# Performance work log

Measured on AMD Instinct MI355X. Metric: run time of the kernel, lower is better.

The kernel has to match this reference:

```python
import jax, jax.numpy as jnp
from jax import lax
import numpy as np

B, T, F, U = 256, 150, 1024, 28


def setup_inputs() -> dict:
    key = jax.random.key(0)
    ks = jax.random.split(key, 10)
    s = 0.05  # keep tanh/sigmoid unsaturated, ~glorot magnitude
    return {
        "x": jax.random.normal(ks[0], (B, T, F), jnp.float32),
        "Wa": jax.random.normal(ks[1], (U, F), jnp.float32) * s,
        "Ua": jax.random.normal(ks[2], (F, F), jnp.float32) * s,
        "Va": jax.random.normal(ks[3], (F, 1), jnp.float32) * s,
        "Ba1": jax.random.normal(ks[4], (1, F), jnp.float32) * s,
        "Ba2": jax.random.normal(ks[5], (1, F), jnp.float32) * s,
        "Ba3": jax.random.normal(ks[6], (1, 1), jnp.float32) * s,
        "gru_kernel": jax.random.normal(ks[7], (F, 3 * U), jnp.float32) * s,
        "gru_rkernel": jax.random.normal(ks[8], (U, 3 * U), jnp.float32) * s,
        "gru_bias": jax.random.normal(ks[9], (2, 3 * U), jnp.float32) * s,
    }


def reference(x, Wa, Ua, Va, Ba1, Ba2, Ba3, gru_kernel, gru_rkernel, gru_bias):
    b, t, f = x.shape
    u = Wa.shape[0]
    # UaH is loop-invariant in the original (x @ Ua + Ba2 each step) -> hoist it.
    UaH = jnp.einsum('btf,fg->btg', x, Ua) + Ba2  # (B,T,F)

    def step(h, _):
        # Bahdanau attention conditioned on previous GRU state h (B,U)
        WaS = h @ Wa + Ba1                                    # (B,F)
        scores = jnp.einsum('btf,fo->bt', jnp.tanh(UaH + WaS[:, None, :]), Va) + Ba3[0, 0]
        a = jax.nn.softmax(scores, axis=1)                    # (B,T)
        ctx = jnp.einsum('btf,bt->bf', x, a)                  # (B,F)
        # Keras GRUCell (reset_after=True)
        xz = ctx @ gru_kernel + gru_bias[0]                   # (B,3U)
        hz = h @ gru_rkernel + gru_bias[1]                    # (B,3U)
        x_z, x_r, x_h = jnp.split(xz, 3, axis=-1)
        r_z, r_r, r_h = jnp.split(hz, 3, axis=-1)
        z = jax.nn.sigmoid(x_z + r_z)
        r = jax.nn.sigmoid(x_r + r_r)
        hh = jnp.tanh(x_h + r * r_h)
        h_new = z * h + (1.0 - z) * hh
        return h_new, h_new

    h0 = jnp.zeros((b, u), x.dtype)
    _, ys = lax.scan(step, h0, None, length=t)  # (T,B,U)
    return jnp.transpose(ys, (1, 0, 2))         # (B,T,U)
```

## Files before the change

### kernel.cpp

```cpp
#include <hip/hip_runtime.h>
#include <hip/hip_bf16.h>


typedef _Float16 h8 __attribute__((ext_vector_type(8)));
typedef _Float16 h4 __attribute__((ext_vector_type(4)));
typedef _Float16 h2 __attribute__((ext_vector_type(2)));
typedef float    f4 __attribute__((ext_vector_type(4)));
typedef float    f2 __attribute__((ext_vector_type(2)));

#define B_   256
#define T_   150
#define F_   1024
#define U_   28
#define TU3  84

__device__ __forceinline__ float fast_exp(float x) {
    return __builtin_amdgcn_exp2f(x * 1.4426950408889634f);
}
__device__ __forceinline__ float fast_tanh(float x) {
    float e = __builtin_amdgcn_exp2f(x * 2.8853900817779268f);
    float r = __builtin_amdgcn_rcpf(e + 1.0f);
    return 1.0f - 2.0f * r;
}
__device__ __forceinline__ float fast_sigmoid(float x) {
    float e = __builtin_amdgcn_exp2f(-x * 1.4426950408889634f);
    return __builtin_amdgcn_rcpf(1.0f + e);
}

__global__ void k_cvt(const float* __restrict__ in, _Float16* __restrict__ out, int n4) {
    int i = blockIdx.x * blockDim.x + threadIdx.x;
    int stride = gridDim.x * blockDim.x;
    const f4* in4 = (const f4*)in;
    h4* out4 = (h4*)out;
    for (; i < n4; i += stride) {
        f4 v = in4[i];
        h4 o;
        o[0] = (_Float16)v[0]; o[1] = (_Float16)v[1];
        o[2] = (_Float16)v[2]; o[3] = (_Float16)v[3];
        out4[i] = o;
    }
}

__global__ void k_cvt_transpose(const float* __restrict__ in, _Float16* __restrict__ out) {
    int idx = blockIdx.x * blockDim.x + threadIdx.x;
    int r = idx >> 10, c = idx & 1023;
    out[(c << 10) + r] = (_Float16)in[idx];
}

#define BM 128
#define BN 128
#define BK 32
#define LDT 40

__global__ __launch_bounds__(256) void k_gemm(
    const _Float16* __restrict__ A,
    const _Float16* __restrict__ Bt,
    const float*    __restrict__ bias,
    _Float16*       __restrict__ C)
{
    __shared__ _Float16 As[BM][LDT];
    __shared__ _Float16 Bs[BN][LDT];
    const int K = 1024;
    int bm = blockIdx.y, bn = blockIdx.x;
    int tid = threadIdx.x;
    int lane = tid & 63, wid = tid >> 6;
    int wm = wid >> 1, wn = wid & 1;
    f4 acc[4][4];
#pragma unroll
    for (int i = 0; i < 4; i++)
#pragma unroll
        for (int j = 0; j < 4; j++) { f4 z = {0.f, 0.f, 0.f, 0.f}; acc[i][j] = z; }

    int row0 = bm * BM, col0 = bn * BN;
    for (int kt = 0; kt < K; kt += BK) {
#pragma unroll
        for (int p = 0; p < 2; ++p) {
            int s = tid + p * 256;
            int r = s >> 2, seg = s & 3;
            h8 va = *(const h8*)(A  + (size_t)(row0 + r) * K + kt + seg * 8);
            *(h8*)(&As[r][seg * 8]) = va;
            h8 vb = *(const h8*)(Bt + (size_t)(col0 + r) * K + kt + seg * 8);
            *(h8*)(&Bs[r][seg * 8]) = vb;
        }
        __syncthreads();
        int kq = (lane >> 4) * 8;
        h8 af[4], bf[4];
#pragma unroll
        for (int mi = 0; mi < 4; mi++) af[mi] = *(const h8*)(&As[wm * 64 + mi * 16 + (lane & 15)][kq]);
#pragma unroll
        for (int ni = 0; ni < 4; ni++) bf[ni] = *(const h8*)(&Bs[wn * 64 + ni * 16 + (lane & 15)][kq]);
#pragma unroll
        for (int mi = 0; mi < 4; mi++)
#pragma unroll
            for (int ni = 0; ni < 4; ni++)
                acc[mi][ni] = __builtin_amdgcn_mfma_f32_16x16x32_f16(af[mi], bf[ni], acc[mi][ni], 0, 0, 0);
        __syncthreads();
    }
    int rq = (lane >> 4) * 4, cq = lane & 15;
#pragma unroll
    for (int mi = 0; mi < 4; mi++)
#pragma unroll
        for (int ni = 0; ni < 4; ni++) {
            int gc = col0 + wn * 64 + ni * 16 + cq;
            float bv = bias[gc];
#pragma unroll
            for (int j = 0; j < 4; j++) {
                int gr = row0 + wm * 64 + mi * 16 + rq + j;
                C[(size_t)gr * 1024 + gc] = (_Float16)(acc[mi][ni][j] + bv);
            }
        }
}

#define XLD 72

__global__ __launch_bounds__(256) void k_gemm_xg(
    const _Float16* __restrict__ A,
    const float*    __restrict__ gk,
    _Float16*       __restrict__ C)
{
    __shared__ _Float16 As[128][XLD];
    __shared__ _Float16 Bs[96][XLD];
    int tid = threadIdx.x;
    int lane = tid & 63, wid = tid >> 6;
    int wm = wid >> 1, wn = wid & 1;
    int row0 = blockIdx.x * 128;
    f4 acc[4][3];
#pragma unroll
    for (int i = 0; i < 4; i++)
#pragma unroll
        for (int j = 0; j < 3; j++) { f4 z = {0.f, 0.f, 0.f, 0.f}; acc[i][j] = z; }

    if (tid < 432) { h2 z; z[0] = (_Float16)0.f; z[1] = (_Float16)0.f; ((h2*)&Bs[84][0])[tid] = z; }

    for (int kt = 0; kt < 1024; kt += 64) {
#pragma unroll
        for (int p = 0; p < 4; ++p) {
            int s = tid + p * 256;
            int r = s >> 3, seg = s & 7;
            *(h8*)(&As[r][seg * 8]) = *(const h8*)(A + (size_t)(row0 + r) * 1024 + kt + seg * 8);
        }
#pragma unroll
        for (int p = 0; p < 21; ++p) {
            int s = tid + p * 256;
            int j = s % 84, k = s / 84;
            Bs[j][k] = (_Float16)gk[(size_t)(kt + k) * 84 + j];
        }
        __syncthreads();
#pragma unroll
        for (int kk = 0; kk < 64; kk += 32) {
            int kq = kk + (lane >> 4) * 8;
            h8 af[4], bf[3];
#pragma unroll
            for (int mi = 0; mi < 4; mi++) af[mi] = *(const h8*)(&As[wm * 64 + mi * 16 + (lane & 15)][kq]);
#pragma unroll
            for (int ni = 0; ni < 3; ni++) bf[ni] = *(const h8*)(&Bs[wn * 48 + ni * 16 + (lane & 15)][kq]);
#pragma unroll
            for (int mi = 0; mi < 4; mi++)
#pragma unroll
                for (int ni = 0; ni < 3; ni++)
                    acc[mi][ni] = __builtin_amdgcn_mfma_f32_16x16x32_f16(af[mi], bf[ni], acc[mi][ni], 0, 0, 0);
        }
        __syncthreads();
    }
    int rq = (lane >> 4) * 4, cq = lane & 15;
#pragma unroll
    for (int mi = 0; mi < 4; mi++)
#pragma unroll
        for (int ni = 0; ni < 3; ni++) {
            int gc = wn * 48 + ni * 16 + cq;
            if (gc < 84) {
#pragma unroll
                for (int j = 0; j < 4; j++) {
                    int gr = row0 + wm * 64 + mi * 16 + rq + j;
                    C[(size_t)gr * 84 + gc] = (_Float16)acc[mi][ni][j];
                }
            }
        }
}

__global__ __launch_bounds__(1024) void k_recur2(
    const _Float16* __restrict__ uah,
    const _Float16* __restrict__ xg,
    const float* __restrict__ Wa,
    const float* __restrict__ Va,
    const float* __restrict__ Ba1,
    const float* __restrict__ grk,
    const float* __restrict__ gbias,
    float* __restrict__ out)
{
    __shared__ _Float16 sWa[U_ * F_];
    __shared__ _Float16 sXG[T_ * TU3];
    __shared__ float sWaS[F_];
    __shared__ float sScore[160];
    __shared__ float sPart[8 * TU3];
    __shared__ float sGrk[U_ * TU3];
    __shared__ float sHz[TU3];
    __shared__ float sH[U_];

    int b = blockIdx.x;
    int tid = threadIdx.x;
    int lane = tid & 63, wvid = tid >> 6;

    for (int i = tid; i < U_ * F_; i += 1024) sWa[i] = (_Float16)Wa[i];
    {
        const _Float16* xgb = xg + (size_t)b * T_ * TU3;
        for (int i = tid; i < T_ * TU3; i += 1024) sXG[i] = xgb[i];
    }
    for (int i = tid; i < U_ * TU3; i += 1024) sGrk[i] = grk[i];
    if (tid < U_) sH[tid] = 0.f;

    float rBa1 = Ba1[tid];
    float rV0[8], rV1[8];
    {
        f4 a0 = *(const f4*)(Va + 8 * lane);
        f4 a1 = *(const f4*)(Va + 8 * lane + 4);
        f4 b0 = *(const f4*)(Va + 512 + 8 * lane);
        f4 b1 = *(const f4*)(Va + 512 + 8 * lane + 4);
#pragma unroll
        for (int e = 0; e < 4; ++e) { rV0[e] = a0[e]; rV0[4 + e] = a1[e]; rV1[e] = b0[e]; rV1[4 + e] = b1[e]; }
    }
    int p4c = tid / TU3, p4j = tid - p4c * TU3;
    bool p4on = tid < 8 * TU3;
    bool hzon = (tid >= 896) && (tid < 896 + TU3);
    int hj = tid - 896;
    float rGb1 = hzon ? gbias[TU3 + hj] : 0.f;
    float rG0 = 0.f, rG1 = 0.f, rG2 = 0.f;
    if (tid < U_) { rG0 = gbias[tid]; rG1 = gbias[U_ + tid]; rG2 = gbias[2 * U_ + tid]; }
    __syncthreads();

    const _Float16* ub = uah + (size_t)b * T_ * F_;
    float* ob = out + (size_t)b * T_ * U_;

    for (int t = 0; t < T_; ++t) {
        {
            float acc = rBa1;
#pragma unroll
            for (int u = 0; u < U_; ++u) acc += sH[u] * (float)sWa[u * F_ + tid];
            sWaS[tid] = acc;
        }
        __syncthreads();
        float rW0[8], rW1[8];
        {
            f4 a0 = *(const f4*)(sWaS + 8 * lane);
            f4 a1 = *(const f4*)(sWaS + 8 * lane + 4);
            f4 b0 = *(const f4*)(sWaS + 512 + 8 * lane);
            f4 b1 = *(const f4*)(sWaS + 512 + 8 * lane + 4);
#pragma unroll
            for (int e = 0; e < 4; ++e) { rW0[e] = a0[e]; rW0[4 + e] = a1[e]; rW1[e] = b0[e]; rW1[4 + e] = b1[e]; }
        }
        {
            int r = wvid;
            const h8* pr = (const h8*)(ub + (size_t)r * F_);
            h8 u0 = pr[lane], u1 = pr[64 + lane];
            while (r < T_) {
                int rn = r + 16;
                h8 n0, n1;
                if (rn < T_) {
                    const h8* pn = (const h8*)(ub + (size_t)rn * F_);
                    n0 = pn[lane]; n1 = pn[64 + lane];
                }
                float acc = 0.f;
#pragma unroll
                for (int e = 0; e < 8; ++e) {
                    float s0 = (float)u0[e] + rW0[e];
                    acc += fast_tanh(s0) * rV0[e];
                    float s1 = (float)u1[e] + rW1[e];
                    acc += fast_tanh(s1) * rV1[e];
                }
#pragma unroll
                for (int off = 32; off; off >>= 1) acc += __shfl_xor(acc, off, 64);
                if (lane == 0) sScore[r] = acc;
                u0 = n0; u1 = n1; r = rn;
            }
        }
        __syncthreads();
        if (wvid == 0) {
            float v0 = (lane < T_)       ? sScore[lane]       : -1e30f;
            float v1 = (lane + 64 < T_)  ? sScore[lane + 64]  : -1e30f;
            float v2 = (lane + 128 < T_) ? sScore[lane + 128] : -1e30f;
            float m = fmaxf(v0, fmaxf(v1, v2));
#pragma unroll
            for (int off = 32; off; off >>= 1) m = fmaxf(m, __shfl_xor(m, off, 64));
            float e0 = (lane < T_)       ? fast_exp(v0 - m) : 0.f;
            float e1 = (lane + 64 < T_)  ? fast_exp(v1 - m) : 0.f;
            float e2 = (lane + 128 < T_) ? fast_exp(v2 - m) : 0.f;
            float s = e0 + e1 + e2;
#pragma unroll
            for (int off = 32; off; off >>= 1) s += __shfl_xor(s, off, 64);
            float rs = __builtin_amdgcn_rcpf(s);
            if (lane < T_)       sScore[lane]       = e0 * rs;
            if (lane + 64 < T_)  sScore[lane + 64]  = e1 * rs;
            if (lane + 128 < T_) sScore[lane + 128] = e2 * rs;
        }
        __syncthreads();
        if (p4on) {
            float acc = 0.f;
            for (int r = p4c; r < T_; r += 8) acc += sScore[r] * (float)sXG[r * TU3 + p4j];
            sPart[p4c * TU3 + p4j] = acc;
        }
        if (hzon) {
            float hz = rGb1;
#pragma unroll
            for (int u = 0; u < U_; ++u) hz += sH[u] * sGrk[u * TU3 + hj];
            sHz[hj] = hz;
        }
        __syncthreads();
        if (tid < U_) {
            float x0 = rG0, x1 = rG1, x2 = rG2;
#pragma unroll
            for (int c = 0; c < 8; ++c) {
                x0 += sPart[c * TU3 + tid];
                x1 += sPart[c * TU3 + U_ + tid];
                x2 += sPart[c * TU3 + 2 * U_ + tid];
            }
            float z  = fast_sigmoid(x0 + sHz[tid]);
            float r  = fast_sigmoid(x1 + sHz[U_ + tid]);
            float hh = fast_tanh(x2 + r * sHz[2 * U_ + tid]);
            float hn = z * sH[tid] + (1.f - z) * hh;
            sH[tid] = hn;
            ob[(size_t)t * U_ + tid] = hn;
        }
        __syncthreads();
    }
}

extern "C" void kernel_launch(void* const* d_in, const int* in_sizes, int n_in,
                              void* d_out, int out_size, void* d_ws, size_t ws_size,
                              hipStream_t stream) {
    (void)in_sizes; (void)n_in; (void)out_size; (void)ws_size;
    const float* x   = (const float*)d_in[0];
    const float* Wa  = (const float*)d_in[1];
    const float* Ua  = (const float*)d_in[2];
    const float* Va  = (const float*)d_in[3];
    const float* Ba1 = (const float*)d_in[4];
    const float* Ba2 = (const float*)d_in[5];
    const float* gk  = (const float*)d_in[7];
    const float* grk = (const float*)d_in[8];
    const float* gb  = (const float*)d_in[9];
    float* out = (float*)d_out;

    const size_t NX = (size_t)B_ * T_ * F_;
    _Float16* xh  = (_Float16*)d_ws;
    _Float16* uat = xh + NX;
    _Float16* uah = uat + (size_t)F_ * F_;
    _Float16* xgh = uah + NX;

    k_cvt<<<2048, 256, 0, stream>>>(x, xh, (int)(NX / 4));
    k_cvt_transpose<<<(F_ * F_) / 256, 256, 0, stream>>>(Ua, uat);
    dim3 gg(F_ / BN, (B_ * T_) / BM);
    k_gemm<<<gg, 256, 0, stream>>>(xh, uat, Ba2, uah);
    k_gemm_xg<<<(B_ * T_) / 128, 256, 0, stream>>>(xh, gk, xgh);
    k_recur2<<<B_, 1024, 0, stream>>>(uah, xgh, Wa, Va, Ba1, grk, gb, out);
}
```

Before: 2.667 ms.

## Fold tanh constants into scores and defer softmax normalization past context reduction

The attention score loop now rewrites tanh·Va as a constant sum minus 2·Va·rcp(exp2+1), with the 2·log2e scale folded into WaS and Va, which trims per-element arithmetic in the hot loop. Softmax drops its max subtraction and separate normalization pass: each score is exponentiated directly, the denominator is summed by a spare wavefront in parallel with the context reduction, and the 1/sum scale is applied to the final small vector. This removes a full barrier phase per timestep. Without max subtraction, exp can overflow if scores grow large, which relies on scores staying bounded.

Measured after the change: 2.231 ms. -16.4%, faster.

```diff
diff --git a/kernel.cpp b/kernel.cpp
--- a/kernel.cpp
+++ b/kernel.cpp
@@ -14,17 +14,20 @@
 #define U_   28
 #define TU3  84
 
+#define C2LOG2E 2.8853900817779268f
+#define LOG2E   1.4426950408889634f
+
 __device__ __forceinline__ float fast_exp(float x) {
-    return __builtin_amdgcn_exp2f(x * 1.4426950408889634f);
+    return __builtin_amdgcn_exp2f(x * LOG2E);
+}
+__device__ __forceinline__ float fast_sigmoid(float x) {
+    float e = __builtin_amdgcn_exp2f(-x * LOG2E);
+    return __builtin_amdgcn_rcpf(1.0f + e);
 }
 __device__ __forceinline__ float fast_tanh(float x) {
-    float e = __builtin_amdgcn_exp2f(x * 2.8853900817779268f);
+    float e = __builtin_amdgcn_exp2f(x * C2LOG2E);
     float r = __builtin_amdgcn_rcpf(e + 1.0f);
     return 1.0f - 2.0f * r;
-}
-__device__ __forceinline__ float fast_sigmoid(float x) {
-    float e = __builtin_amdgcn_exp2f(-x * 1.4426950408889634f);
-    return __builtin_amdgcn_rcpf(1.0f + e);
 }
 
 __global__ void k_cvt(const float* __restrict__ in, _Float16* __restrict__ out, int n4) {
@@ -196,6 +199,7 @@
     __shared__ float sGrk[U_ * TU3];
     __shared__ float sHz[TU3];
     __shared__ float sH[U_];
+    __shared__ float sDen;
 
     int b = blockIdx.x;
     int tid = threadIdx.x;
@@ -210,17 +214,22 @@
     if (tid < U_) sH[tid] = 0.f;
 
     float rBa1 = Ba1[tid];
-    float rV0[8], rV1[8];
+    float rA0[8], rA1[8], vaBase = 0.f;
     {
         f4 a0 = *(const f4*)(Va + 8 * lane);
         f4 a1 = *(const f4*)(Va + 8 * lane + 4);
         f4 b0 = *(const f4*)(Va + 512 + 8 * lane);
         f4 b1 = *(const f4*)(Va + 512 + 8 * lane + 4);
 #pragma unroll
-        for (int e = 0; e < 4; ++e) { rV0[e] = a0[e]; rV0[4 + e] = a1[e]; rV1[e] = b0[e]; rV1[4 + e] = b1[e]; }
+        for (int e = 0; e < 4; ++e) {
+            rA0[e] = -2.f * a0[e]; rA0[4 + e] = -2.f * a1[e];
+            rA1[e] = -2.f * b0[e]; rA1[4 + e] = -2.f * b1[e];
+            vaBase += a0[e] + a1[e] + b0[e] + b1[e];
+        }
     }
     int p4c = tid / TU3, p4j = tid - p4c * TU3;
     bool p4on = tid < 8 * TU3;
+    bool denon = (wvid == 13);
     bool hzon = (tid >= 896) && (tid < 896 + TU3);
     int hj = tid - 896;
     float rGb1 = hzon ? gbias[TU3 + hj] : 0.f;
@@ -246,7 +255,10 @@
             f4 b0 = *(const f4*)(sWaS + 512 + 8 * lane);
             f4 b1 = *(const f4*)(sWaS + 512 + 8 * lane + 4);
 #pragma unroll
-            for (int e = 0; e < 4; ++e) { rW0[e] = a0[e]; rW0[4 + e] = a1[e]; rW1[e] = b0[e]; rW1[4 + e] = b1[e]; }
+            for (int e = 0; e < 4; ++e) {
+                rW0[e] = a0[e] * C2LOG2E; rW0[4 + e] = a1[e] * C2LOG2E;
+                rW1[e] = b0[e] * C2LOG2E; rW1[4 + e] = b1[e] * C2LOG2E;
+            }
         }
         {
             int r = wvid;
@@ -259,44 +271,37 @@
                     const h8* pn = (const h8*)(ub + (size_t)rn * F_);
                     n0 = pn[lane]; n1 = pn[64 + lane];
                 }
-                float acc = 0.f;
+                float acc = vaBase;
 #pragma unroll
                 for (int e = 0; e < 8; ++e) {
-                    float s0 = (float)u0[e] + rW0[e];
-                    acc += fast_tanh(s0) * rV0[e];
-                    float s1 = (float)u1[e] + rW1[e];
-                    acc += fast_tanh(s1) * rV1[e];
+                    float t0 = fmaf((float)u0[e], C2LOG2E, rW0[e]);
+                    float r0 = __builtin_amdgcn_rcpf(__builtin_amdgcn_exp2f(t0) + 1.0f);
+                    acc = fmaf(rA0[e], r0, acc);
+                    float t1 = fmaf((float)u1[e], C2LOG2E, rW1[e]);
+                    float r1 = __builtin_amdgcn_rcpf(__builtin_amdgcn_exp2f(t1) + 1.0f);
+                    acc = fmaf(rA1[e], r1, acc);
                 }
 #pragma unroll
                 for (int off = 32; off; off >>= 1) acc += __shfl_xor(acc, off, 64);
-                if (lane == 0) sScore[r] = acc;
+                if (lane == 0) sScore[r] = fast_exp(acc);
                 u0 = n0; u1 = n1; r = rn;
             }
-        }
-        __syncthreads();
-        if (wvid == 0) {
-            float v0 = (lane < T_)       ? sScore[lane]       : -1e30f;
-            float v1 = (lane + 64 < T_)  ? sScore[lane + 64]  : -1e30f;
-            float v2 = (lane + 128 < T_) ? sScore[lane + 128] : -1e30f;
-            float m = fmaxf(v0, fmaxf(v1, v2));
-#pragma unroll
-            for (int off = 32; off; off >>= 1) m = fmaxf(m, __shfl_xor(m, off, 64));
-            float e0 = (lane < T_)       ? fast_exp(v0 - m) : 0.f;
-            float e1 = (lane + 64 < T_)  ? fast_exp(v1 - m) : 0.f;
-            float e2 = (lane + 128 < T_) ? fast_exp(v2 - m) : 0.f;
-            float s = e0 + e1 + e2;
-#pragma unroll
-            for (int off = 32; off; off >>= 1) s += __shfl_xor(s, off, 64);
-            float rs = __builtin_amdgcn_rcpf(s);
-            if (lane < T_)       sScore[lane]       = e0 * rs;
-            if (lane + 64 < T_)  sScore[lane + 64]  = e1 * rs;
-            if (lane + 128 < T_) sScore[lane + 128] = e2 * rs;
         }
         __syncthreads();
         if (p4on) {
             float acc = 0.f;
-            for (int r = p4c; r < T_; r += 8) acc += sScore[r] * (float)sXG[r * TU3 + p4j];
+            for (int r = p4c; r < T_; r += 8)
+                acc = fmaf((float)sXG[r * TU3 + p4j], sScore[r], acc);
             sPart[p4c * TU3 + p4j] = acc;
+        }
+        if (denon) {
+            float d0 = (lane < T_)       ? sScore[lane]       : 0.f;
+            float d1 = (lane + 64 < T_)  ? sScore[lane + 64]  : 0.f;
+            float d2 = (lane + 128 < T_) ? sScore[lane + 128] : 0.f;
+            float ds = d0 + d1 + d2;
+#pragma unroll
+            for (int off = 32; off; off >>= 1) ds += __shfl_xor(ds, off, 64);
+            if (lane == 0) sDen = ds;
         }
         if (hzon) {
             float hz = rGb1;
@@ -306,13 +311,17 @@
         }
         __syncthreads();
         if (tid < U_) {
-            float x0 = rG0, x1 = rG1, x2 = rG2;
+            float rs = __builtin_amdgcn_rcpf(sDen);
+            float x0 = 0.f, x1 = 0.f, x2 = 0.f;
 #pragma unroll
             for (int c = 0; c < 8; ++c) {
                 x0 += sPart[c * TU3 + tid];
                 x1 += sPart[c * TU3 + U_ + tid];
                 x2 += sPart[c * TU3 + 2 * U_ + tid];
             }
+            x0 = fmaf(x0, rs, rG0);
+            x1 = fmaf(x1, rs, rG1);
+            x2 = fmaf(x2, rs, rG2);
             float z  = fast_sigmoid(x0 + sHz[tid]);
             float r  = fast_sigmoid(x1 + sHz[U_ + tid]);
             float hh = fast_tanh(x2 + r * sHz[2 * U_ + tid]);
```
